# Kernel optimization log

Hardware: AMD Instinct MI355X
Metric: run time of the kernel (lower is better)

## Reference

```python
import jax, jax.numpy as jnp
import numpy as np

NUM_CLASSES = 80
S = 7            # grid_size
NB = 2           # num_boxes per cell
LAMBDA_COORD = 5.0
LAMBDA_NOOBJ = 0.5
N_BOX = 20       # padded boxes per image


def setup_inputs() -> dict:
    key = jax.random.key(0)
    k1, k2, k3, k4 = jax.random.split(key, 4)
    B = 4096
    predictions = jax.random.uniform(k1, (B, S, S, NB, 5 + NUM_CLASSES), dtype=jnp.float32)
    # build valid normalized xyxy boxes: centers in [0.1,0.9], half-sizes in [0.01,0.085]
    centers = jax.random.uniform(k2, (B, N_BOX, 2), dtype=jnp.float32) * 0.8 + 0.1
    half = jax.random.uniform(k3, (B, N_BOX, 2), dtype=jnp.float32) * 0.075 + 0.01
    targets_boxes = jnp.concatenate([centers - half, centers + half], axis=-1)
    targets_labels = jax.random.randint(k4, (B, N_BOX), 0, NUM_CLASSES)
    return {"predictions": predictions, "targets_boxes": targets_boxes, "targets_labels": targets_labels}


def encode_targets(boxes, labels):
    # boxes: [B,N,4] xyxy normalized; labels: [B,N] int
    B, N, _ = boxes.shape
    x = (boxes[..., 0] + boxes[..., 2]) * 0.5
    y = (boxes[..., 1] + boxes[..., 3]) * 0.5
    w = boxes[..., 2] - boxes[..., 0]
    h = boxes[..., 3] - boxes[..., 1]
    j = jnp.clip(jnp.floor(x * S).astype(jnp.int32), 0, S - 1)
    i = jnp.clip(jnp.floor(y * S).astype(jnp.int32), 0, S - 1)
    x_cell = x * S - j
    y_cell = y * S - i
    onehot = jax.nn.one_hot(labels, NUM_CLASSES, dtype=boxes.dtype)
    feats = jnp.concatenate([x_cell[..., None], y_cell[..., None], w[..., None], h[..., None],
                             jnp.ones_like(x_cell)[..., None], onehot], axis=-1)  # [B,N,5+C]
    bidx = jnp.arange(B, dtype=jnp.int32)[:, None]
    flat = ((bidx * S + i) * S + j).ravel()                       # [B*N] cell ids
    order = jnp.broadcast_to(jnp.arange(N, dtype=jnp.int32), (B, N)).ravel()
    winner = jnp.full((B * S * S,), N, dtype=jnp.int32).at[flat].min(order)
    cell_b = jnp.arange(B * S * S, dtype=jnp.int32) // (S * S)
    sel = jnp.minimum(winner, N - 1)
    grid = feats[cell_b, sel]
    grid = jnp.where((winner < N)[:, None], grid, jnp.zeros_like(grid))
    return grid.reshape(B, S, S, 5 + NUM_CLASSES)


def iou_xywh(a, b):
    ax1 = a[..., 0] - a[..., 2] * 0.5; ay1 = a[..., 1] - a[..., 3] * 0.5
    ax2 = a[..., 0] + a[..., 2] * 0.5; ay2 = a[..., 1] + a[..., 3] * 0.5
    bx1 = b[..., 0] - b[..., 2] * 0.5; by1 = b[..., 1] - b[..., 3] * 0.5
    bx2 = b[..., 0] + b[..., 2] * 0.5; by2 = b[..., 1] + b[..., 3] * 0.5
    iw = jnp.clip(jnp.minimum(ax2, bx2) - jnp.maximum(ax1, bx1), 0.0)
    ih = jnp.clip(jnp.minimum(ay2, by2) - jnp.maximum(ay1, by1), 0.0)
    inter = iw * ih
    union = (ax2 - ax1) * (ay2 - ay1) + (bx2 - bx1) * (by2 - by1) - inter
    return inter / (union + 1e-6)


def yolo_loss(predictions, targets_boxes, targets_labels):
    B = predictions.shape[0]
    tg = encode_targets(targets_boxes, targets_labels)   # [B,S,S,5+C]
    txy, twh = tg[..., :2], tg[..., 2:4]
    tconf, tcls = tg[..., 4:5], tg[..., 5:]
    obj = (tconf[..., 0] > 0).astype(predictions.dtype)   # [B,S,S]
    # responsible box = argmax IoU per cell, masked by obj
    pred_boxes = predictions[..., 0:4]                     # [B,S,S,NB,4]
    tgt_boxes = jnp.concatenate([txy, twh], axis=-1)[:, :, :, None, :]
    ious = iou_xywh(pred_boxes, jnp.broadcast_to(tgt_boxes, pred_boxes.shape))  # [B,S,S,NB]
    best = jnp.argmax(ious, axis=-1)
    resp = jax.nn.one_hot(best, NB, dtype=predictions.dtype) * obj[..., None]   # [B,S,S,NB]
    pxy = predictions[..., 0:2]; pwh = predictions[..., 2:4]
    pconf = predictions[..., 4:5]; pcls = predictions[..., 5:]
    om = obj[..., None, None]        # [B,S,S,1,1]
    rm = resp[..., None]             # [B,S,S,NB,1]
    loss_xy = LAMBDA_COORD * jnp.sum(om * rm * (pxy - txy[:, :, :, None, :]) ** 2) / B
    loss_wh = LAMBDA_COORD * jnp.sum(om * rm * (jnp.sqrt(jnp.clip(pwh, 1e-6)) - jnp.sqrt(jnp.clip(twh[:, :, :, None, :], 1e-6))) ** 2) / B
    loss_conf_obj = jnp.sum(om * rm * (pconf - tconf[:, :, :, None, :]) ** 2) / B
    loss_conf_noobj = LAMBDA_NOOBJ * jnp.sum((1.0 - obj)[..., None, None] * pconf ** 2) / B
    pred_cls_resp = jnp.sum(pcls * rm, axis=3)             # [B,S,S,C]
    loss_cls = jnp.sum(obj[..., None] * (pred_cls_resp - tcls) ** 2) / B
    return loss_xy + loss_wh + loss_conf_obj + loss_conf_noobj + loss_cls


def reference(predictions, targets_boxes, targets_labels):
    return yolo_loss(predictions, targets_boxes, targets_labels)
```

## Files before the change

kernel.cpp:

```cpp
#include <hip/hip_runtime.h>

#define S 7
#define NB 2
#define NC 80
#define NBOX 20
#define CELLS 49
#define CH 85
#define PAIR 170
#define PER_B 8330
#define NIMG 4096
#define NCELL_TOT (NIMG*CELLS)
#define NBOXSLOT (NIMG*CELLS*NB)
#define N4TOT (NIMG*PER_B/4)
#define PREP_BLOCKS (NCELL_TOT/256)
#define STREAM_BLOCKS 1960
#define STREAM_ITERS 17
#define L_COORD 5.0f
#define L_NOOBJ 0.5f
#define INV_B (1.0f/4096.0f)

typedef float vfloat4 __attribute__((ext_vector_type(4)));

__device__ __forceinline__ void block_reduce_atomic(float acc, float* out)
{
    __shared__ float s_wsum[4];
    int tid = threadIdx.x;
    #pragma unroll
    for (int off = 32; off > 0; off >>= 1) acc += __shfl_down(acc, off, 64);
    int lane = tid & 63, wv = tid >> 6;
    if (lane == 0) s_wsum[wv] = acc;
    __syncthreads();
    if (tid == 0)
        atomicAdd(out, (s_wsum[0] + s_wsum[1] + s_wsum[2] + s_wsum[3]) * INV_B);
}

__global__ __launch_bounds__(256) void prep_kernel(
    const float* __restrict__ pred,
    const float* __restrict__ boxes,
    const int*   __restrict__ labels,
    float2*      __restrict__ wb2,
    float*       __restrict__ out)
{
    const int tid   = threadIdx.x;
    const int gcell = blockIdx.x * 256 + tid;
    const unsigned img = (unsigned)gcell / (unsigned)CELLS;
    const int cell  = gcell - (int)img * CELLS;

    const float* bx = boxes + (size_t)img * NBOX * 4;
    int winner = NBOX;
    float wx = 0.f, wy = 0.f, wwd = 0.f, wht = 0.f;
    #pragma unroll 4
    for (int b = NBOX - 1; b >= 0; --b) {
        float x1 = bx[4*b], y1 = bx[4*b+1], x2 = bx[4*b+2], y2 = bx[4*b+3];
        float x = (x1 + x2) * 0.5f, y = (y1 + y2) * 0.5f;
        int j = min(max((int)floorf(x * (float)S), 0), S - 1);
        int i = min(max((int)floorf(y * (float)S), 0), S - 1);
        if (i * S + j == cell) {
            winner = b; wx = x; wy = y; wwd = x2 - x1; wht = y2 - y1;
        }
    }

    const float* p = pred + (size_t)gcell * PAIR;
    float acc;
    float2 w;
    if (winner < NBOX) {
        int i = cell / S, j = cell - (cell / S) * S;
        float tx = wx * (float)S - (float)j;
        float ty = wy * (float)S - (float)i;
        float tw = wwd, th = wht;

        float bx1 = tx - tw * 0.5f, by1 = ty - th * 0.5f;
        float bx2 = tx + tw * 0.5f, by2 = ty + th * 0.5f;
        float barea = (bx2 - bx1) * (by2 - by1);
        float iou[2], px[2], py[2], pw[2], ph[2];
        #pragma unroll
        for (int nb = 0; nb < NB; nb++) {
            px[nb] = p[nb * CH + 0]; py[nb] = p[nb * CH + 1];
            pw[nb] = p[nb * CH + 2]; ph[nb] = p[nb * CH + 3];
            float ax1 = px[nb] - pw[nb] * 0.5f, ay1 = py[nb] - ph[nb] * 0.5f;
            float ax2 = px[nb] + pw[nb] * 0.5f, ay2 = py[nb] + ph[nb] * 0.5f;
            float iw = fmaxf(fminf(ax2, bx2) - fmaxf(ax1, bx1), 0.0f);
            float ih = fmaxf(fminf(ay2, by2) - fmaxf(ay1, by1), 0.0f);
            float inter = iw * ih;
            float uni = (ax2 - ax1) * (ay2 - ay1) + barea - inter;
            iou[nb] = inter / (uni + 1e-6f);
        }
        int resp = (iou[1] > iou[0]) ? 1 : 0;
        w = (resp == 0) ? make_float2(1.f, 0.f) : make_float2(0.f, 1.f);

        int lab = labels[img * NBOX + winner];
        float pc = p[resp * CH + 4];
        float pl = p[resp * CH + 5 + lab];
        float dx = px[resp] - tx, dy = py[resp] - ty;
        float dw = sqrtf(fmaxf(pw[resp], 1e-6f)) - sqrtf(fmaxf(tw, 1e-6f));
        float dh = sqrtf(fmaxf(ph[resp], 1e-6f)) - sqrtf(fmaxf(th, 1e-6f));
        acc = L_COORD * (dx * dx + dy * dy + dw * dw + dh * dh)
            + (1.0f - 2.0f * pc)
            + (1.0f - 2.0f * pl)
            - (px[resp] * px[resp] + py[resp] * py[resp]
             + pw[resp] * pw[resp] + ph[resp] * ph[resp]);
    } else {
        float c0 = p[4], c1 = p[CH + 4];
        acc = L_NOOBJ * (c0 * c0 + c1 * c1);
        w = make_float2(0.f, 0.f);
    }
    wb2[gcell] = w;
    block_reduce_atomic(acc, out);
}

__global__ __launch_bounds__(256) void stream_kernel(
    const vfloat4* __restrict__ p4,
    const float*   __restrict__ wb,
    float*         __restrict__ out)
{
    const int tid  = threadIdx.x;
    const int base = blockIdx.x * (STREAM_ITERS * 256);

    float acc = 0.0f;
    #pragma unroll
    for (int k = 0; k < STREAM_ITERS; ++k) {
        int e = base + k * 256 + tid;
        vfloat4 v = p4[e];
        unsigned ff = 4u * (unsigned)e;
        unsigned bi = ff / 85u;
        int r85 = (int)(ff - bi * 85u);
        int thr = 85 - r85;
        float wa = wb[bi];
        float wn = wb[bi + 1];
        float w1 = (1 < thr) ? wa : wn;
        float w2 = (2 < thr) ? wa : wn;
        float w3 = (3 < thr) ? wa : wn;
        acc += wa * (v.x * v.x);
        acc += w1 * (v.y * v.y);
        acc += w2 * (v.z * v.z);
        acc += w3 * (v.w * v.w);
    }
    block_reduce_atomic(acc, out);
}

extern "C" void kernel_launch(void* const* d_in, const int* in_sizes, int n_in,
                              void* d_out, int out_size, void* d_ws, size_t ws_size,
                              hipStream_t stream) {
    const float* pred   = (const float*)d_in[0];
    const float* boxes  = (const float*)d_in[1];
    const int*   labels = (const int*)d_in[2];
    float* out = (float*)d_out;

    float* wb = (float*)d_ws;

    hipMemsetAsync(d_out, 0, sizeof(float) * out_size, stream);
    prep_kernel<<<PREP_BLOCKS, 256, 0, stream>>>(pred, boxes, labels,
                                                 (float2*)wb, out);
    stream_kernel<<<STREAM_BLOCKS, 256, 0, stream>>>((const vfloat4*)pred, wb, out);
}
```

Measured before the change: 219.0 us.

## Fuse prep and stream kernels into one wave-per-image loss kernel

Replaces the two-kernel design (per-cell prep writing responsibility weights, then a flat streaming pass over predictions) with a single kernel where each wavefront handles one image. Box-to-cell assignment is done with a ballot across lanes holding the boxes, and the 170 floats of each cell are loaded once with scalar per-lane loads. This removes the workspace round-trip, the second launch and the redundant re-read of coordinate and confidence values. In exchange, loads are scalar rather than float4, only 1024 blocks are launched, and the per-cell loop carries a serial chain of shuffles and IoU math per wave.

Result: slower. 627.7 us (+186.6%).

```diff
diff --git a/kernel.cpp b/kernel.cpp
--- a/kernel.cpp
+++ b/kernel.cpp
@@ -9,147 +9,120 @@
 #define PAIR 170
 #define PER_B 8330
 #define NIMG 4096
-#define NCELL_TOT (NIMG*CELLS)
-#define NBOXSLOT (NIMG*CELLS*NB)
-#define N4TOT (NIMG*PER_B/4)
-#define PREP_BLOCKS (NCELL_TOT/256)
-#define STREAM_BLOCKS 1960
-#define STREAM_ITERS 17
+#define IMGS_PER_BLOCK 4
+#define GRID (NIMG/IMGS_PER_BLOCK)
 #define L_COORD 5.0f
 #define L_NOOBJ 0.5f
 #define INV_B (1.0f/4096.0f)
 
-typedef float vfloat4 __attribute__((ext_vector_type(4)));
+__global__ __launch_bounds__(256) void fused_kernel(
+    const float*  __restrict__ pred,
+    const float4* __restrict__ boxes4,
+    const int*    __restrict__ labels,
+    float*        __restrict__ out)
+{
+    const int tid  = threadIdx.x;
+    const int lane = tid & 63;
+    const int wv   = tid >> 6;
+    const int img  = blockIdx.x * IMGS_PER_BLOCK + wv;
 
-__device__ __forceinline__ void block_reduce_atomic(float acc, float* out)
-{
-    __shared__ float s_wsum[4];
-    int tid = threadIdx.x;
+    float cx = 0.f, cy = 0.f, bw = 0.f, bh = 0.f;
+    int myCell = -1, myLab = 0;
+    if (lane < NBOX) {
+        float4 bq = boxes4[img * NBOX + lane];
+        cx = (bq.x + bq.z) * 0.5f; cy = (bq.y + bq.w) * 0.5f;
+        bw = bq.z - bq.x;          bh = bq.w - bq.y;
+        int j = min(max((int)floorf(cx * (float)S), 0), S - 1);
+        int i = min(max((int)floorf(cy * (float)S), 0), S - 1);
+        myCell = i * S + j;
+        myLab  = labels[img * NBOX + lane];
+    }
+
+    float acc = 0.f;
+    const float* pc = pred + (size_t)img * PER_B;
+
+    #pragma unroll 2
+    for (int c = 0; c < CELLS; ++c, pc += PAIR) {
+        float p0a = pc[lane];
+        float p0b = pc[CH + lane];
+        float p1a = (lane < CH - 64) ? pc[64 + lane]      : 0.f;
+        float p1b = (lane < CH - 64) ? pc[CH + 64 + lane] : 0.f;
+
+        unsigned long long mask = __ballot(myCell == c);
+        bool obj = (mask != 0ULL);
+        int win = __ffsll(mask) - 1;
+        win = (win < 0) ? 0 : win;
+
+        float tx = __shfl(cx, win) * (float)S - (float)(c % S);
+        float ty = __shfl(cy, win) * (float)S - (float)(c / S);
+        float tw = __shfl(bw, win);
+        float th = __shfl(bh, win);
+        int  lab = __shfl(myLab, win);
+
+        float px0 = __shfl(p0a, 0), py0 = __shfl(p0a, 1);
+        float pw0 = __shfl(p0a, 2), ph0 = __shfl(p0a, 3);
+        float px1 = __shfl(p0b, 0), py1 = __shfl(p0b, 1);
+        float pw1 = __shfl(p0b, 2), ph1 = __shfl(p0b, 3);
+
+        float bx1 = tx - tw * 0.5f, by1 = ty - th * 0.5f;
+        float bx2 = tx + tw * 0.5f, by2 = ty + th * 0.5f;
+        float barea = (bx2 - bx1) * (by2 - by1);
+
+        float a0x1 = px0 - pw0 * 0.5f, a0y1 = py0 - ph0 * 0.5f;
+        float a0x2 = px0 + pw0 * 0.5f, a0y2 = py0 + ph0 * 0.5f;
+        float iw0 = fmaxf(fminf(a0x2, bx2) - fmaxf(a0x1, bx1), 0.f);
+        float ih0 = fmaxf(fminf(a0y2, by2) - fmaxf(a0y1, by1), 0.f);
+        float inter0 = iw0 * ih0;
+        float iou0 = inter0 / ((a0x2 - a0x1) * (a0y2 - a0y1) + barea - inter0 + 1e-6f);
+
+        float a1x1 = px1 - pw1 * 0.5f, a1y1 = py1 - ph1 * 0.5f;
+        float a1x2 = px1 + pw1 * 0.5f, a1y2 = py1 + ph1 * 0.5f;
+        float iw1 = fmaxf(fminf(a1x2, bx2) - fmaxf(a1x1, bx1), 0.f);
+        float ih1 = fmaxf(fminf(a1y2, by2) - fmaxf(a1y1, by1), 0.f);
+        float inter1 = iw1 * ih1;
+        float iou1 = inter1 / ((a1x2 - a1x1) * (a1y2 - a1y1) + barea - inter1 + 1e-6f);
+
+        bool resp1 = (iou1 > iou0);
+
+        float pa = resp1 ? p0b : p0a;
+        int ch = lane;
+        float t = (ch >= 5) ? (((ch - 5) == lab) ? 1.f : 0.f)
+                : (ch == 4) ? 1.f
+                : (ch == 0) ? tx : (ch == 1) ? ty : (ch == 2) ? tw : th;
+        bool issq = (ch == 2) || (ch == 3);
+        float q  = issq ? sqrtf(fmaxf(pa, 1e-6f)) : pa;
+        float tq = issq ? sqrtf(fmaxf(t,  1e-6f)) : t;
+        float d0 = q - tq;
+        float m0 = (ch < 4) ? L_COORD : 1.f;
+        float objc = m0 * d0 * d0;
+
+        float pb = resp1 ? p1b : p1a;
+        float t1 = ((59 + lane) == lab) ? 1.f : 0.f;
+        float d1 = pb - t1;
+        objc += (lane < CH - 64) ? d1 * d1 : 0.f;
+
+        float noc = (ch == 4) ? L_NOOBJ * (p0a * p0a + p0b * p0b) : 0.f;
+
+        acc += obj ? objc : noc;
+    }
+
     #pragma unroll
     for (int off = 32; off > 0; off >>= 1) acc += __shfl_down(acc, off, 64);
-    int lane = tid & 63, wv = tid >> 6;
+    __shared__ float s_wsum[IMGS_PER_BLOCK];
     if (lane == 0) s_wsum[wv] = acc;
     __syncthreads();
     if (tid == 0)
         atomicAdd(out, (s_wsum[0] + s_wsum[1] + s_wsum[2] + s_wsum[3]) * INV_B);
 }
 
-__global__ __launch_bounds__(256) void prep_kernel(
-    const float* __restrict__ pred,
-    const float* __restrict__ boxes,
-    const int*   __restrict__ labels,
-    float2*      __restrict__ wb2,
-    float*       __restrict__ out)
-{
-    const int tid   = threadIdx.x;
-    const int gcell = blockIdx.x * 256 + tid;
-    const unsigned img = (unsigned)gcell / (unsigned)CELLS;
-    const int cell  = gcell - (int)img * CELLS;
-
-    const float* bx = boxes + (size_t)img * NBOX * 4;
-    int winner = NBOX;
-    float wx = 0.f, wy = 0.f, wwd = 0.f, wht = 0.f;
-    #pragma unroll 4
-    for (int b = NBOX - 1; b >= 0; --b) {
-        float x1 = bx[4*b], y1 = bx[4*b+1], x2 = bx[4*b+2], y2 = bx[4*b+3];
-        float x = (x1 + x2) * 0.5f, y = (y1 + y2) * 0.5f;
-        int j = min(max((int)floorf(x * (float)S), 0), S - 1);
-        int i = min(max((int)floorf(y * (float)S), 0), S - 1);
-        if (i * S + j == cell) {
-            winner = b; wx = x; wy = y; wwd = x2 - x1; wht = y2 - y1;
-        }
-    }
-
-    const float* p = pred + (size_t)gcell * PAIR;
-    float acc;
-    float2 w;
-    if (winner < NBOX) {
-        int i = cell / S, j = cell - (cell / S) * S;
-        float tx = wx * (float)S - (float)j;
-        float ty = wy * (float)S - (float)i;
-        float tw = wwd, th = wht;
-
-        float bx1 = tx - tw * 0.5f, by1 = ty - th * 0.5f;
-        float bx2 = tx + tw * 0.5f, by2 = ty + th * 0.5f;
-        float barea = (bx2 - bx1) * (by2 - by1);
-        float iou[2], px[2], py[2], pw[2], ph[2];
-        #pragma unroll
-        for (int nb = 0; nb < NB; nb++) {
-            px[nb] = p[nb * CH + 0]; py[nb] = p[nb * CH + 1];
-            pw[nb] = p[nb * CH + 2]; ph[nb] = p[nb * CH + 3];
-            float ax1 = px[nb] - pw[nb] * 0.5f, ay1 = py[nb] - ph[nb] * 0.5f;
-            float ax2 = px[nb] + pw[nb] * 0.5f, ay2 = py[nb] + ph[nb] * 0.5f;
-            float iw = fmaxf(fminf(ax2, bx2) - fmaxf(ax1, bx1), 0.0f);
-            float ih = fmaxf(fminf(ay2, by2) - fmaxf(ay1, by1), 0.0f);
-            float inter = iw * ih;
-            float uni = (ax2 - ax1) * (ay2 - ay1) + barea - inter;
-            iou[nb] = inter / (uni + 1e-6f);
-        }
-        int resp = (iou[1] > iou[0]) ? 1 : 0;
-        w = (resp == 0) ? make_float2(1.f, 0.f) : make_float2(0.f, 1.f);
-
-        int lab = labels[img * NBOX + winner];
-        float pc = p[resp * CH + 4];
-        float pl = p[resp * CH + 5 + lab];
-        float dx = px[resp] - tx, dy = py[resp] - ty;
-        float dw = sqrtf(fmaxf(pw[resp], 1e-6f)) - sqrtf(fmaxf(tw, 1e-6f));
-        float dh = sqrtf(fmaxf(ph[resp], 1e-6f)) - sqrtf(fmaxf(th, 1e-6f));
-        acc = L_COORD * (dx * dx + dy * dy + dw * dw + dh * dh)
-            + (1.0f - 2.0f * pc)
-            + (1.0f - 2.0f * pl)
-            - (px[resp] * px[resp] + py[resp] * py[resp]
-             + pw[resp] * pw[resp] + ph[resp] * ph[resp]);
-    } else {
-        float c0 = p[4], c1 = p[CH + 4];
-        acc = L_NOOBJ * (c0 * c0 + c1 * c1);
-        w = make_float2(0.f, 0.f);
-    }
-    wb2[gcell] = w;
-    block_reduce_atomic(acc, out);
-}
-
-__global__ __launch_bounds__(256) void stream_kernel(
-    const vfloat4* __restrict__ p4,
-    const float*   __restrict__ wb,
-    float*         __restrict__ out)
-{
-    const int tid  = threadIdx.x;
-    const int base = blockIdx.x * (STREAM_ITERS * 256);
-
-    float acc = 0.0f;
-    #pragma unroll
-    for (int k = 0; k < STREAM_ITERS; ++k) {
-        int e = base + k * 256 + tid;
-        vfloat4 v = p4[e];
-        unsigned ff = 4u * (unsigned)e;
-        unsigned bi = ff / 85u;
-        int r85 = (int)(ff - bi * 85u);
-        int thr = 85 - r85;
-        float wa = wb[bi];
-        float wn = wb[bi + 1];
-        float w1 = (1 < thr) ? wa : wn;
-        float w2 = (2 < thr) ? wa : wn;
-        float w3 = (3 < thr) ? wa : wn;
-        acc += wa * (v.x * v.x);
-        acc += w1 * (v.y * v.y);
-        acc += w2 * (v.z * v.z);
-        acc += w3 * (v.w * v.w);
-    }
-    block_reduce_atomic(acc, out);
-}
-
 extern "C" void kernel_launch(void* const* d_in, const int* in_sizes, int n_in,
                               void* d_out, int out_size, void* d_ws, size_t ws_size,
                               hipStream_t stream) {
-    const float* pred   = (const float*)d_in[0];
-    const float* boxes  = (const float*)d_in[1];
-    const int*   labels = (const int*)d_in[2];
+    const float*  pred   = (const float*)d_in[0];
+    const float4* boxes4 = (const float4*)d_in[1];
+    const int*    labels = (const int*)d_in[2];
     float* out = (float*)d_out;
 
-    float* wb = (float*)d_ws;
-
     hipMemsetAsync(d_out, 0, sizeof(float) * out_size, stream);
-    prep_kernel<<<PREP_BLOCKS, 256, 0, stream>>>(pred, boxes, labels,
-                                                 (float2*)wb, out);
-    stream_kernel<<<STREAM_BLOCKS, 256, 0, stream>>>((const vfloat4*)pred, wb, out);
+    fused_kernel<<<GRID, 256, 0, stream>>>(pred, boxes4, labels, out);
 }
```
